# Optimization experiments

Hardware: AMD Instinct MI355X
Metric: run time of the kernel (lower is better)

Reference implementation:

```python
import jax, jax.numpy as jnp
import numpy as np
import math

B = 32; N = 512000; D = 64; NENT = 100000; NEDGE = 1000000; NREL = 200
K_SOURCE = 100; K_MIN = 50; K_MAX = 1000; L_INFL = 4; A_SLOPE = 1.0
TEMP = 1.0; LAM_NOISE = 1.0; COS_EPS = 1e-8


def compute_topk(l):
    # sigmoid schedule for layer-dependent Top-K (python ints, trace-time)
    if l < L_INFL:
        s = 1.0 / (1.0 + math.exp(-A_SLOPE * (l - L_INFL / 2)))
        return int(K_SOURCE + (K_MAX - K_SOURCE) * s)
    s = 1.0 / (1.0 + math.exp(-A_SLOPE * (l - 3 * L_INFL / 2)))
    return int(K_MIN + (K_MAX - K_MIN) * (1.0 - s))


def setup_inputs():
    key = jax.random.key(0)
    k = jax.random.split(key, 14)
    i = jnp.arange(N)
    b = i % B                     # batches interleaved -> every batch has diff nodes
    e = (i // B) * 6 + b          # unique entity per (batch, node), max < NENT
    nodes = jnp.stack([b, e], axis=1)
    return {
        "hidden": jax.random.normal(k[0], (N, D), jnp.float32),
        "nodes": nodes,
        "scores": jax.random.uniform(k[1], (N,), jnp.float32) + 0.1,
        "h0": jax.random.normal(k[2], (1, N, D), jnp.float32),
        "alpha": jax.random.normal(k[3], (NEDGE, 1), jnp.float32),
        "hidden_q": jax.random.normal(k[4], (B, D), jnp.float32),
        "q_rel": jax.random.randint(k[5], (B,), 0, 2 * NREL + 1),
        "edges": jax.random.randint(k[6], (NEDGE, 6), 0, N),
        "old_nodes_new_idx": jnp.arange(N // 2),
        "batch_size": B,
        "message": jax.random.normal(k[7], (NEDGE, D), jnp.float32),
        "obj": jax.random.randint(k[8], (NEDGE,), 0, N),
        "alpha_temp": jax.random.normal(k[9], (NEDGE, 1), jnp.float32),
        "l": 2,
        "noise": jax.random.normal(k[10], (N, 3), jnp.float32),
        "mlp_w1": jax.random.normal(k[11], (2 * D, D), jnp.float32) * 0.05,
        "mlp_b1": jnp.zeros((D,), jnp.float32),
        "mlp_w2": jax.random.normal(k[12], (D, D), jnp.float32) * 0.05,
        "mlp_b2": jnp.zeros((D,), jnp.float32),
        "rel_embed": jax.random.normal(k[13], (2 * NREL + 1, D), jnp.float32) * 0.05,
        "expert_emb": jax.random.normal(jax.random.fold_in(key, 1), (3, D), jnp.float32),
        "w_n": jax.random.normal(jax.random.fold_in(key, 2), (D,), jnp.float32) * 0.05,
    }


def _dense_topk_mult(vals, bidx, eidx, diff, K, B_):
    # scatter per-diff-node values into dense [B, n_ent], softmax over entities,
    # top-K hard mask, straight-through multiplier (hard - sg(p) + p) on diff nodes.
    neg = jnp.float32(-jnp.inf)
    dense = jnp.full((B_, NENT), neg, jnp.float32).at[bidx, eidx].set(jnp.where(diff, vals, neg))
    probs = jax.nn.softmax(dense, axis=1)
    _, idx = jax.lax.top_k(probs, K)
    hard = jnp.zeros((B_, NENT), bool).at[jnp.arange(B_)[:, None], idx].set(True)
    p = probs[bidx, eidx]
    h = hard[bidx, eidx].astype(jnp.float32)
    return jnp.where(diff, h - jax.lax.stop_gradient(p) + p, 1.0)


def _forward(hidden, scores, h0, hidden_q, alpha_temp, mlp_w1, mlp_b1, mlp_w2, mlp_b2,
             rel_embed, expert_emb, w_n, nodes, q_rel, edges, old_nodes_new_idx,
             batch_size, noise, l):
    bidx = nodes[:, 0]
    eidx = nodes[:, 1]
    # ---- noisy gate over 3 pruning experts ----
    q_rel_e = rel_embed[q_rel]                                   # [B, D]
    ctx_in = jnp.concatenate([hidden_q[bidx], q_rel_e[bidx]], axis=-1)  # [N, 2D]
    ctx = jax.nn.relu(ctx_in @ mlp_w1 + mlp_b1) @ mlp_w2 + mlp_b2       # [N, D]
    escore = ctx @ expert_emb.T                                  # [N, 3]
    nscale = jax.nn.softplus(ctx @ w_n)[:, None]                 # [N, 1]
    escore = escore + LAM_NOISE * noise * nscale
    weights = jax.nn.softmax(escore / TEMP, axis=-1)             # [N, 3]
    importance = weights.sum(0) / weights.sum()                  # [3], sums to 1
    w = importance  # num_pruning_experts=3: topk over all 3 + renorm is identity

    diff = jnp.ones((N,), bool).at[old_nodes_new_idx].set(False)
    K_l = compute_topk(l)

    # expert 0: score-based pruner
    m0 = _dense_topk_mult(scores, bidx, eidx, diff, K_l, batch_size)

    # expert 1: cosine-similarity pruner (hidden vs query relation embedding)
    qn = q_rel_e[bidx]
    num = (hidden * qn).sum(-1)
    den = jnp.maximum(jnp.linalg.norm(hidden, axis=-1), COS_EPS) * \
          jnp.maximum(jnp.linalg.norm(qn, axis=-1), COS_EPS)
    m1 = _dense_topk_mult(num / den, bidx, eidx, diff, K_l, batch_size)

    # expert 2: alpha pruner -- segment-max of edge attention onto target nodes,
    # softmax over the global node dim, top-K among new nodes only.
    obj_e = edges[:, 5]
    mx = jax.ops.segment_max(alpha_temp[:, 0], obj_e, num_segments=N)
    node_probs = jax.nn.softmax(mx / TEMP)
    masked = jnp.where(diff, node_probs, -1.0)   # probs >= 0, so topk lands on diff
    _, top_i = jax.lax.top_k(masked, K_l)
    hard2 = jnp.zeros((N,), bool).at[top_i].set(True)
    m2 = jnp.where(diff, hard2.astype(jnp.float32) - jax.lax.stop_gradient(node_probs) + node_probs, 1.0)

    # ---- combine: each expert returns the full node set with diff rows rescaled,
    # and the hashed node-id lookup is the identity permutation here, so the
    # index_add combine reduces to a weighted sum of multipliers. ----
    wm = w[0] * m0 + w[1] * m1 + w[2] * m2                        # [N]
    hidden_c = hidden * wm[:, None]
    scores_c = scores * wm
    h0_c = h0 * wm[None, :, None]

    cv = jnp.std(weights, ddof=1) / (weights.mean() + 1e-5)       # torch unbiased std
    L_imp = cv ** 2
    return hidden_c, scores_c, h0_c, L_imp


def reference(hidden, nodes, scores, h0, alpha, hidden_q, q_rel, edges,
              old_nodes_new_idx, batch_size, message, obj, alpha_temp, l, noise,
              mlp_w1, mlp_b1, mlp_w2, mlp_b2, rel_embed, expert_emb, w_n):
    # alpha / message / obj are passed through in the original but unused in the
    # computed path; the final scores!=0 row filter is replaced by keeping the
    # full (zero-preserving) arrays to stay jit-compatible.
    return _forward(hidden, scores, h0, hidden_q, alpha_temp, mlp_w1, mlp_b1,
                    mlp_w2, mlp_b2, rel_embed, expert_emb, w_n, nodes, q_rel,
                    edges, old_nodes_new_idx, batch_size, noise, l)
```

## Files before the change

### kernel.cpp

```cpp
#include <hip/hip_runtime.h>
#include <stdint.h>
#include <math.h>

#define DD 64
#define K_SOURCE_C 100
#define K_MIN_C 50
#define K_MAX_C 1000
#define L_INFL_C 4
#define A_SLOPE_C 1.0
#define COS_EPS_C 1e-8f
#define NBINS 8192
#define CAPC 3584
#define NHB 192
#define NWB 1024

__device__ __forceinline__ uint32_t f2mono(float f) {
    uint32_t u = __float_as_uint(f);
    return (u & 0x80000000u) ? ~u : (u | 0x80000000u);
}

__constant__ int c_shifts[5] = {51, 38, 25, 12, 0};
__constant__ int c_nbits[5]  = {13, 13, 13, 13, 12};

__global__ void initctx_kernel(uint32_t* mx, uint8_t* diff, int* cnt,
                               int* Kp, int* node_cnt, uint32_t* ghist, const int* l_ptr,
                               const float* hidden_q, const int* q_rel, const float* rel_embed,
                               const float* w1, const float* b1, const float* w2, const float* b2,
                               const float* expert_emb, const float* w_n,
                               float* escore, float* nscale, float* qvec, float* qnorm,
                               int N, int B, int nb) {
    int blk = blockIdx.x, t = threadIdx.x;
    if (blk < nb) {
        int i = blk * 256 + t;
        if (i < N) { mx[i] = 0u; diff[i] = 1; }
        if (i < B) cnt[i] = 0;
        if (i < NBINS) ghist[i] = 0u;
        if (i == 0) {
            *node_cnt = 0;
            double l = (double)(*l_ptr);
            int K;
            if (l < (double)L_INFL_C) {
                double s = 1.0 / (1.0 + exp(-A_SLOPE_C * (l - L_INFL_C / 2.0)));
                K = (int)(K_SOURCE_C + (K_MAX_C - K_SOURCE_C) * s);
            } else {
                double s = 1.0 / (1.0 + exp(-A_SLOPE_C * (l - 3.0 * L_INFL_C / 2.0)));
                K = (int)(K_MIN_C + (K_MAX_C - K_MIN_C) * (1.0 - s));
            }
            *Kp = K;
        }
        return;
    }
    int b = blk - nb;
    if (b >= B) return;
    __shared__ float cin[2 * DD];
    __shared__ float h1s[DD];
    float qv = 0.f;
    if (t < DD) {
        int q = q_rel[b];
        qv = rel_embed[(size_t)q * DD + t];
        qvec[b * DD + t] = qv;
        cin[t] = hidden_q[b * DD + t];
        cin[DD + t] = qv;
    }
    __syncthreads();
    if (t < DD) {
        float acc = b1[t];
        for (int j = 0; j < 2 * DD; j++) acc += cin[j] * w1[j * DD + t];
        h1s[t] = fmaxf(acc, 0.f);
    }
    __syncthreads();
    if (t < DD) {
        float c = b2[t];
        for (int j = 0; j < DD; j++) c += h1s[j] * w2[j * DD + t];
        float e0 = c * expert_emb[0 * DD + t];
        float e1 = c * expert_emb[1 * DD + t];
        float e2 = c * expert_emb[2 * DD + t];
        float wn = c * w_n[t];
        float qq = qv * qv;
        for (int m = 32; m >= 1; m >>= 1) {
            e0 += __shfl_xor(e0, m); e1 += __shfl_xor(e1, m); e2 += __shfl_xor(e2, m);
            wn += __shfl_xor(wn, m); qq += __shfl_xor(qq, m);
        }
        if (t == 0) {
            escore[b * 3 + 0] = e0; escore[b * 3 + 1] = e1; escore[b * 3 + 2] = e2;
            nscale[b] = fmaxf(wn, 0.f) + log1pf(expf(-fabsf(wn)));
            qnorm[b] = fmaxf(sqrtf(qq), COS_EPS_C);
        }
    }
}

__global__ void segdiff_kernel(const int* edges, const float* alpha_temp, uint32_t* mx,
                               uint8_t* diff, const int* old_idx,
                               int NE, int n_old, int N, int eb) {
    int blk = blockIdx.x, t = threadIdx.x;
    if (blk < eb) {
        int e = blk * 256 + t;
        if (e < NE) {
            int o = edges[(size_t)e * 6 + 5];
            if (o >= 0 && o < N) atomicMax(&mx[o], f2mono(alpha_temp[e]));
        }
    } else {
        int j = (blk - eb) * 256 + t;
        if (j < n_old) {
            int idx = old_idx[j];
            if (idx >= 0 && idx < N) diff[idx] = 0;
        }
    }
}

__global__ void nodewc_kernel(const float* hidden, const int* nodes, const float* noise,
                              const float* qvec, const float* qnorm,
                              const float* escore, const float* nscale,
                              float* cosvals, double* partials, int N, int B) {
    int t = threadIdx.x;
    int sub = t & 15;
    double s0 = 0, s1 = 0, s2 = 0, sq = 0;
    int ngroups = (N + 15) >> 4;
    for (int g = blockIdx.x; g < ngroups; g += gridDim.x) {
        int node = g * 16 + (t >> 4);
        if (node < N) {
            int b = nodes[2 * node];
            bool bv = (b >= 0 && b < B);
            float4 h4 = *(const float4*)(hidden + (size_t)node * DD + sub * 4);
            float num = 0.f;
            if (bv) {
                float4 q4 = *(const float4*)(qvec + b * DD + sub * 4);
                num = h4.x * q4.x + h4.y * q4.y + h4.z * q4.z + h4.w * q4.w;
            }
            float hs = h4.x * h4.x + h4.y * h4.y + h4.z * h4.z + h4.w * h4.w;
            for (int m = 8; m >= 1; m >>= 1) { num += __shfl_xor(num, m); hs += __shfl_xor(hs, m); }
            if (sub == 0) {
                float qn = bv ? qnorm[b] : COS_EPS_C;
                cosvals[node] = num / (fmaxf(sqrtf(hs), COS_EPS_C) * qn);
                if (bv) {
                    float ns = nscale[b];
                    float e0 = escore[b * 3 + 0] + noise[3 * node + 0] * ns;
                    float e1 = escore[b * 3 + 1] + noise[3 * node + 1] * ns;
                    float e2 = escore[b * 3 + 2] + noise[3 * node + 2] * ns;
                    float mm = fmaxf(e0, fmaxf(e1, e2));
                    float x0 = expf(e0 - mm), x1 = expf(e1 - mm), x2 = expf(e2 - mm);
                    float s = x0 + x1 + x2;
                    x0 /= s; x1 /= s; x2 /= s;
                    s0 += x0; s1 += x1; s2 += x2;
                    sq += (double)x0 * x0 + (double)x1 * x1 + (double)x2 * x2;
                }
            }
        }
    }
    for (int m = 32; m >= 1; m >>= 1) {
        s0 += __shfl_xor(s0, m); s1 += __shfl_xor(s1, m);
        s2 += __shfl_xor(s2, m); sq += __shfl_xor(sq, m);
    }
    __shared__ double red[4][4];
    int wid = t >> 6, lane = t & 63;
    if (lane == 0) { red[wid][0] = s0; red[wid][1] = s1; red[wid][2] = s2; red[wid][3] = sq; }
    __syncthreads();
    if (t == 0) {
        double a0 = 0, a1 = 0, a2 = 0, a3 = 0;
        for (int w = 0; w < 4; w++) { a0 += red[w][0]; a1 += red[w][1]; a2 += red[w][2]; a3 += red[w][3]; }
        partials[blockIdx.x * 4 + 0] = a0;
        partials[blockIdx.x * 4 + 1] = a1;
        partials[blockIdx.x * 4 + 2] = a2;
        partials[blockIdx.x * 4 + 3] = a3;
    }
}

__global__ void compactstats_kernel(const int* nodes, const uint8_t* diff, const float* scores,
                                    const float* cosvals, const uint32_t* mx,
                                    uint64_t* keys0, uint64_t* keys1, uint64_t* nkeys,
                                    int* cnt, int* node_cnt,
                                    const double* partials, float* wvec, float* out_L,
                                    int N, int B, int CAP, int nb) {
    int blk = blockIdx.x, t = threadIdx.x;
    if (blk == nb) {
        double s0 = 0, s1 = 0, s2 = 0, sq = 0;
        for (int i = t; i < NWB; i += 256) {
            s0 += partials[4 * i + 0]; s1 += partials[4 * i + 1];
            s2 += partials[4 * i + 2]; sq += partials[4 * i + 3];
        }
        for (int m = 32; m >= 1; m >>= 1) {
            s0 += __shfl_xor(s0, m); s1 += __shfl_xor(s1, m);
            s2 += __shfl_xor(s2, m); sq += __shfl_xor(sq, m);
        }
        __shared__ double red[4][4];
        int wid = t >> 6, lane = t & 63;
        if (lane == 0) { red[wid][0] = s0; red[wid][1] = s1; red[wid][2] = s2; red[wid][3] = sq; }
        __syncthreads();
        if (t == 0) {
            double c0 = 0, c1 = 0, c2 = 0, S2 = 0;
            for (int w = 0; w < 4; w++) { c0 += red[w][0]; c1 += red[w][1]; c2 += red[w][2]; S2 += red[w][3]; }
            double tot = c0 + c1 + c2;
            wvec[0] = (float)(c0 / tot); wvec[1] = (float)(c1 / tot); wvec[2] = (float)(c2 / tot);
            double n = 3.0 * (double)N;
            double mean = tot / n;
            double var = (S2 - tot * tot / n) / (n - 1.0);
            if (var < 0) var = 0;
            double cv = sqrt(var) / (mean + 1e-5);
            *out_L = (float)(cv * cv);
        }
        return;
    }
    __shared__ int lcnt[64];
    __shared__ int lbase[64];
    __shared__ int nloc_cnt, nloc_base;
    if (t < B) lcnt[t] = 0;
    if (t == 0) nloc_cnt = 0;
    __syncthreads();
    int i = blk * 256 + t;
    int b = -1, loc = 0, nl = 0;
    bool isdiff = (i < N) && diff[i];
    if (isdiff) {
        nl = atomicAdd(&nloc_cnt, 1);
        int bb = nodes[2 * i];
        if (bb >= 0 && bb < B) { b = bb; loc = atomicAdd(&lcnt[b], 1); }
    }
    __syncthreads();
    if (t < B) lbase[t] = lcnt[t] ? atomicAdd(&cnt[t], lcnt[t]) : 0;
    if (t == 0) nloc_base = nloc_cnt ? atomicAdd(node_cnt, nloc_cnt) : 0;
    __syncthreads();
    if (isdiff) {
        nkeys[nloc_base + nl] = ((uint64_t)mx[i] << 32) | (uint64_t)(0xFFFFFFFFu - (uint32_t)i);
        if (b >= 0) {
            int pos = lbase[b] + loc;
            if (pos < CAP) {
                int ei = nodes[2 * i + 1];
                uint64_t tb = (uint64_t)(0xFFFFFFFFu - (uint32_t)ei);
                keys0[(size_t)b * CAP + pos] = ((uint64_t)f2mono(scores[i]) << 32) | tb;
                keys1[(size_t)b * CAP + pos] = ((uint64_t)f2mono(cosvals[i]) << 32) | tb;
            }
        }
    }
}

struct PickScratch { uint32_t wtot[16]; int fd; uint32_t fK; uint32_t total; };

__device__ void block_pick(const uint32_t* hist, int nbins, uint32_t Kr, PickScratch* sc) {
    int t = threadIdx.x;
    int PB = nbins >> 10;
    int lane = t & 63, wid = t >> 6;
    uint32_t csum = 0;
    for (int j = 0; j < PB; j++) csum += hist[PB * t + j];
    uint32_t ssum = csum;
    for (int off = 1; off < 64; off <<= 1) {
        uint32_t v = __shfl_down(ssum, off, 64);
        if (lane + off < 64) ssum += v;
    }
    if (lane == 0) sc->wtot[wid] = ssum;
    if (t == 0) sc->fd = -1;
    __syncthreads();
    uint32_t above = 0, total = 0;
#pragma unroll
    for (int w = 0; w < 16; w++) {
        uint32_t v = sc->wtot[w];
        total += v;
        if (w > wid) above += v;
    }
    uint32_t gcnt = ssum + above - csum;
    int fd = -1; uint32_t fK = 0;
    for (int j = PB - 1; j >= 0; j--) {
        uint32_t h = hist[PB * t + j];
        if (h && gcnt < Kr && gcnt + h >= Kr) { fd = PB * t + j; fK = Kr - gcnt; }
        gcnt += h;
    }
    if (fd >= 0) { sc->fd = fd; sc->fK = fK; }
    if (t == 0) sc->total = total;
    __syncthreads();
}

__global__ __launch_bounds__(1024)
void selA_kernel(const uint64_t* keys0, const uint64_t* keys1, const int* cnt,
                 const uint64_t* nkeys, const int* node_cnt, uint32_t* ghist,
                 uint64_t* T, const int* Kp, int B, int CAP) {
    __shared__ uint32_t hist[NBINS];
    __shared__ PickScratch sc;
    int t = threadIdx.x;
    int blk = blockIdx.x;
    if (blk < 2 * B) {
        int row = (blk < B) ? blk : blk - B;
        const uint64_t* list = ((blk < B) ? keys0 : keys1) + (size_t)row * CAP;
        int n = min(cnt[row], CAP);
        int K = *Kp;
        if (n <= K) { if (t == 0) T[blk] = 0ull; return; }
        uint64_t pref = 0ull;
        uint32_t Kr = (uint32_t)K;
        for (int lev = 0; lev < 5; lev++) {
            int nb = 1 << c_nbits[lev];
            for (int j = t; j < nb; j += 1024) hist[j] = 0;
            __syncthreads();
            uint64_t pmask = (lev == 0) ? 0ull : (~0ull << c_shifts[lev - 1]);
            int sh = c_shifts[lev];
            uint32_t bmask = (uint32_t)(nb - 1);
            for (int i = t; i < n; i += 1024) {
                uint64_t key = list[i];
                if ((key & pmask) == pref)
                    atomicAdd(&hist[(uint32_t)(key >> sh) & bmask], 1u);
            }
            __syncthreads();
            block_pick(hist, nb, Kr, &sc);
            if (sc.fd < 0) { if (t == 0) T[blk] = 0ull; return; }
            pref |= ((uint64_t)sc.fd) << sh;
            Kr = sc.fK;
            __syncthreads();
        }
        if (t == 0) T[blk] = pref;
    } else {
        int nb = blk - 2 * B;
        for (int j = t; j < NBINS; j += 1024) hist[j] = 0;
        __syncthreads();
        int n = *node_cnt;
        for (int i = nb * 1024 + t; i < n; i += NHB * 1024)
            atomicAdd(&hist[(uint32_t)(nkeys[i] >> 51)], 1u);
        __syncthreads();
        for (int j = t; j < NBINS; j += 1024) {
            uint32_t v = hist[j];
            if (v) atomicAdd(&ghist[j], v);
        }
    }
}

__global__ __launch_bounds__(1024)
void selB_kernel(const uint64_t* nkeys, const int* node_cnt, const uint32_t* ghist,
                 uint64_t* T, const int* Kp, int B) {
    __shared__ uint32_t hist[NBINS];
    __shared__ uint64_t cand[CAPC];
    __shared__ PickScratch sc;
    __shared__ int ccnt;
    int t = threadIdx.x;
    int K = *Kp;
    int n = *node_cnt;
    for (int j = t; j < NBINS; j += 1024) hist[j] = ghist[j];
    __syncthreads();
    block_pick(hist, NBINS, (uint32_t)K, &sc);
    if (sc.total <= (uint32_t)K || sc.fd < 0) { if (t == 0) T[2 * B] = 0ull; return; }
    int fd0 = sc.fd;
    uint64_t pref = ((uint64_t)fd0) << 51;
    uint32_t Kr = sc.fK;
    if (t == 0) ccnt = 0;
    __syncthreads();
    for (int i = t; i < n; i += 1024) {
        uint64_t key = nkeys[i];
        if ((int)(key >> 51) == fd0) {
            int p = atomicAdd(&ccnt, 1);
            if (p < CAPC) cand[p] = key;
        }
    }
    __syncthreads();
    int m = ccnt;
    bool inlds = (m <= CAPC);
    if (!inlds) m = n;
    for (int lev = 1; lev < 5; lev++) {
        int nb = 1 << c_nbits[lev];
        for (int j = t; j < nb; j += 1024) hist[j] = 0;
        __syncthreads();
        uint64_t pmask = ~0ull << c_shifts[lev - 1];
        int sh = c_shifts[lev];
        uint32_t bmask = (uint32_t)(nb - 1);
        for (int i = t; i < m; i += 1024) {
            uint64_t key = inlds ? cand[i] : nkeys[i];
            if ((key & pmask) == pref)
                atomicAdd(&hist[(uint32_t)(key >> sh) & bmask], 1u);
        }
        __syncthreads();
        block_pick(hist, nb, Kr, &sc);
        if (sc.fd < 0) { if (t == 0) T[2 * B] = 0ull; return; }
        pref |= ((uint64_t)sc.fd) << sh;
        Kr = sc.fK;
        __syncthreads();
    }
    if (t == 0) T[2 * B] = pref;
}

__global__ void final_kernel(const float* hidden, const float* h0, const float* scores,
                             const int* nodes, const uint8_t* diff, const float* cosvals,
                             const uint32_t* mx, const uint64_t* T, const float* wvec,
                             float* out_hidden, float* out_scores, float* out_h0,
                             int N, int B) {
    int t = threadIdx.x;
    int node = blockIdx.x * 16 + (t >> 4);
    int sub = t & 15;
    bool ok = node < N;
    float wm = 0.f;
    float sc0 = 0.f;
    if (ok && sub == 0) {
        float w0 = wvec[0], w1 = wvec[1], w2 = wvec[2];
        sc0 = scores[node];
        if (!diff[node]) {
            wm = w0 + w1 + w2;
        } else {
            int b = nodes[2 * node];
            int ei = nodes[2 * node + 1];
            float m0 = 0.f, m1 = 0.f;
            if (b >= 0 && b < B) {
                uint64_t tb = (uint64_t)(0xFFFFFFFFu - (uint32_t)ei);
                uint64_t k0 = ((uint64_t)f2mono(sc0) << 32) | tb;
                uint64_t k1 = ((uint64_t)f2mono(cosvals[node]) << 32) | tb;
                m0 = (k0 >= T[b]) ? 1.f : 0.f;
                m1 = (k1 >= T[B + b]) ? 1.f : 0.f;
            }
            uint64_t k2 = ((uint64_t)mx[node] << 32) | (uint64_t)(0xFFFFFFFFu - (uint32_t)node);
            float m2 = (k2 >= T[2 * B]) ? 1.f : 0.f;
            wm = w0 * m0 + w1 * m1 + w2 * m2;
        }
    }
    wm = __shfl(wm, (t & 63) & ~15, 64);
    if (!ok) return;
    size_t off = (size_t)node * DD + sub * 4;
    float4 h4 = *(const float4*)(hidden + off);
    float4 g4 = *(const float4*)(h0 + off);
    float4 o1, o2;
    o1.x = h4.x * wm; o1.y = h4.y * wm; o1.z = h4.z * wm; o1.w = h4.w * wm;
    o2.x = g4.x * wm; o2.y = g4.y * wm; o2.z = g4.z * wm; o2.w = g4.w * wm;
    *(float4*)(out_hidden + off) = o1;
    *(float4*)(out_h0 + off) = o2;
    if (sub == 0) out_scores[node] = sc0 * wm;
}

extern "C" void kernel_launch(void* const* d_in, const int* in_sizes, int n_in,
                              void* d_out, int out_size, void* d_ws, size_t ws_size,
                              hipStream_t stream) {
    const float* hidden     = (const float*)d_in[0];
    const int*   nodes      = (const int*)d_in[1];
    const float* scores     = (const float*)d_in[2];
    const float* h0         = (const float*)d_in[3];
    const float* hidden_q   = (const float*)d_in[5];
    const int*   q_rel      = (const int*)d_in[6];
    const int*   edges      = (const int*)d_in[7];
    const int*   old_idx    = (const int*)d_in[8];
    const float* alpha_temp = (const float*)d_in[12];
    const int*   l_ptr      = (const int*)d_in[13];
    const float* noise      = (const float*)d_in[14];
    const float* mw1        = (const float*)d_in[15];
    const float* mb1        = (const float*)d_in[16];
    const float* mw2        = (const float*)d_in[17];
    const float* mb2        = (const float*)d_in[18];
    const float* rel_embed  = (const float*)d_in[19];
    const float* expert_emb = (const float*)d_in[20];
    const float* w_n        = (const float*)d_in[21];

    int N     = in_sizes[2];
    int NE    = in_sizes[12];
    int n_old = in_sizes[8];
    int B     = in_sizes[5] / DD;
    int CAP   = N / B;
    int nsel  = 2 * B + 1;

    size_t off = 0;
    auto take = [&](size_t bytes) -> size_t {
        size_t p = off; off += (bytes + 15) & ~(size_t)15; return p;
    };
    char* wsb = (char*)d_ws;
    float*    cosvals  = (float*)   (wsb + take((size_t)N * 4));
    uint32_t* mx       = (uint32_t*)(wsb + take((size_t)N * 4));
    uint8_t*  diff     = (uint8_t*) (wsb + take((size_t)N));
    int*      cnt      = (int*)     (wsb + take((size_t)B * 4));
    double*   partials = (double*)  (wsb + take((size_t)NWB * 4 * 8));
    int*      Kp       = (int*)     (wsb + take(16));
    int*      node_cnt = (int*)     (wsb + take(16));
    float*    escore   = (float*)   (wsb + take((size_t)B * 3 * 4));
    float*    nscale   = (float*)   (wsb + take((size_t)B * 4));
    float*    qvec     = (float*)   (wsb + take((size_t)B * DD * 4));
    float*    qnorm    = (float*)   (wsb + take((size_t)B * 4));
    float*    wvec     = (float*)   (wsb + take(16));
    uint64_t* T        = (uint64_t*)(wsb + take((size_t)nsel * 8));
    uint32_t* ghist    = (uint32_t*)(wsb + take((size_t)NBINS * 4));
    size_t keys_bytes  = (size_t)B * CAP * 8;
    size_t nkeys_bytes = (size_t)N * 8;
    uint64_t *keys0, *keys1, *nkeys;
    if (ws_size >= off + 2 * keys_bytes + nkeys_bytes) {
        keys0 = (uint64_t*)(wsb + take(keys_bytes));
        keys1 = (uint64_t*)(wsb + take(keys_bytes));
        nkeys = (uint64_t*)(wsb + take(nkeys_bytes));
    } else {
        keys0 = (uint64_t*)d_out;
        keys1 = keys0 + (size_t)B * CAP;
        nkeys = keys1 + (size_t)B * CAP;
    }

    float* out_hidden = (float*)d_out;
    float* out_scores = out_hidden + (size_t)N * DD;
    float* out_h0     = out_scores + N;
    float* out_L      = out_h0 + (size_t)N * DD;

    int nb = (N + 255) / 256;
    int eb = (NE + 255) / 256;
    int ob = (n_old + 255) / 256;

    initctx_kernel<<<nb + B, 256, 0, stream>>>(mx, diff, cnt, Kp, node_cnt, ghist, l_ptr,
                                               hidden_q, q_rel, rel_embed, mw1, mb1, mw2, mb2,
                                               expert_emb, w_n, escore, nscale, qvec, qnorm,
                                               N, B, nb);
    segdiff_kernel<<<eb + ob, 256, 0, stream>>>(edges, alpha_temp, mx, diff, old_idx,
                                                NE, n_old, N, eb);
    nodewc_kernel<<<NWB, 256, 0, stream>>>(hidden, nodes, noise, qvec, qnorm,
                                           escore, nscale, cosvals, partials, N, B);
    compactstats_kernel<<<nb + 1, 256, 0, stream>>>(nodes, diff, scores, cosvals, mx,
                                                    keys0, keys1, nkeys, cnt, node_cnt,
                                                    partials, wvec, out_L, N, B, CAP, nb);
    selA_kernel<<<2 * B + NHB, 1024, 0, stream>>>(keys0, keys1, cnt, nkeys, node_cnt,
                                                  ghist, T, Kp, B, CAP);
    selB_kernel<<<1, 1024, 0, stream>>>(nkeys, node_cnt, ghist, T, Kp, B);
    final_kernel<<<(N + 15) / 16, 256, 0, stream>>>(hidden, h0, scores, nodes, diff, cosvals,
                                                    mx, T, wvec, out_hidden, out_scores, out_h0, N, B);
}
```

Before: 823.4 us.

## Merge segdiff into nodewc and fold selB into selA via last-block tail

Merges the edge max/diff-marking kernel with the node cosine/weight kernel into a single prep launch that uses block-range dispatch. It also fuses the two selection kernels: every block increments a done counter, and the last block to finish runs the global-histogram threshold pick. This cuts two kernel launches and the gaps between them. The cost is extra shared memory in the fused selection kernel (the candidate buffer), which may lower occupancy, plus a dependence on threadfence/atomic ordering being correct.

```diff
diff --git a/kernel.cpp b/kernel.cpp
--- a/kernel.cpp
+++ b/kernel.cpp
@@ -23,7 +23,8 @@
 __constant__ int c_nbits[5]  = {13, 13, 13, 13, 12};
 
 __global__ void initctx_kernel(uint32_t* mx, uint8_t* diff, int* cnt,
-                               int* Kp, int* node_cnt, uint32_t* ghist, const int* l_ptr,
+                               int* Kp, int* node_cnt, uint32_t* ghist, uint32_t* done_ctr,
+                               const int* l_ptr,
                                const float* hidden_q, const int* q_rel, const float* rel_embed,
                                const float* w1, const float* b1, const float* w2, const float* b2,
                                const float* expert_emb, const float* w_n,
@@ -37,6 +38,7 @@
         if (i < NBINS) ghist[i] = 0u;
         if (i == 0) {
             *node_cnt = 0;
+            *done_ctr = 0u;
             double l = (double)(*l_ptr);
             int K;
             if (l < (double)L_INFL_C) {
@@ -89,34 +91,35 @@
     }
 }
 
-__global__ void segdiff_kernel(const int* edges, const float* alpha_temp, uint32_t* mx,
-                               uint8_t* diff, const int* old_idx,
-                               int NE, int n_old, int N, int eb) {
+__global__ void prep_kernel(const float* hidden, const int* nodes, const float* noise,
+                            const float* qvec, const float* qnorm,
+                            const float* escore, const float* nscale,
+                            float* cosvals, double* partials,
+                            const int* edges, const float* alpha_temp, uint32_t* mx,
+                            uint8_t* diff, const int* old_idx,
+                            int N, int NE, int n_old, int B, int eb) {
     int blk = blockIdx.x, t = threadIdx.x;
-    if (blk < eb) {
-        int e = blk * 256 + t;
-        if (e < NE) {
-            int o = edges[(size_t)e * 6 + 5];
-            if (o >= 0 && o < N) atomicMax(&mx[o], f2mono(alpha_temp[e]));
-        }
-    } else {
-        int j = (blk - eb) * 256 + t;
-        if (j < n_old) {
-            int idx = old_idx[j];
-            if (idx >= 0 && idx < N) diff[idx] = 0;
-        }
-    }
-}
-
-__global__ void nodewc_kernel(const float* hidden, const int* nodes, const float* noise,
-                              const float* qvec, const float* qnorm,
-                              const float* escore, const float* nscale,
-                              float* cosvals, double* partials, int N, int B) {
-    int t = threadIdx.x;
+    if (blk >= NWB) {
+        int rb = blk - NWB;
+        if (rb < eb) {
+            int e = rb * 256 + t;
+            if (e < NE) {
+                int o = edges[(size_t)e * 6 + 5];
+                if (o >= 0 && o < N) atomicMax(&mx[o], f2mono(alpha_temp[e]));
+            }
+        } else {
+            int j = (rb - eb) * 256 + t;
+            if (j < n_old) {
+                int idx = old_idx[j];
+                if (idx >= 0 && idx < N) diff[idx] = 0;
+            }
+        }
+        return;
+    }
     int sub = t & 15;
     double s0 = 0, s1 = 0, s2 = 0, sq = 0;
     int ngroups = (N + 15) >> 4;
-    for (int g = blockIdx.x; g < ngroups; g += gridDim.x) {
+    for (int g = blk; g < ngroups; g += NWB) {
         int node = g * 16 + (t >> 4);
         if (node < N) {
             int b = nodes[2 * node];
@@ -158,10 +161,10 @@
     if (t == 0) {
         double a0 = 0, a1 = 0, a2 = 0, a3 = 0;
         for (int w = 0; w < 4; w++) { a0 += red[w][0]; a1 += red[w][1]; a2 += red[w][2]; a3 += red[w][3]; }
-        partials[blockIdx.x * 4 + 0] = a0;
-        partials[blockIdx.x * 4 + 1] = a1;
-        partials[blockIdx.x * 4 + 2] = a2;
-        partials[blockIdx.x * 4 + 3] = a3;
+        partials[blk * 4 + 0] = a0;
+        partials[blk * 4 + 1] = a1;
+        partials[blk * 4 + 2] = a2;
+        partials[blk * 4 + 3] = a3;
     }
 }
 
@@ -268,11 +271,14 @@
 }
 
 __global__ __launch_bounds__(1024)
-void selA_kernel(const uint64_t* keys0, const uint64_t* keys1, const int* cnt,
-                 const uint64_t* nkeys, const int* node_cnt, uint32_t* ghist,
-                 uint64_t* T, const int* Kp, int B, int CAP) {
+void selAB_kernel(const uint64_t* keys0, const uint64_t* keys1, const int* cnt,
+                  const uint64_t* nkeys, const int* node_cnt, uint32_t* ghist,
+                  uint64_t* T, const int* Kp, uint32_t* done_ctr, int B, int CAP) {
     __shared__ uint32_t hist[NBINS];
+    __shared__ uint64_t cand[CAPC];
     __shared__ PickScratch sc;
+    __shared__ int ccnt;
+    __shared__ int is_tail;
     int t = threadIdx.x;
     int blk = blockIdx.x;
     if (blk < 2 * B) {
@@ -280,29 +286,34 @@
         const uint64_t* list = ((blk < B) ? keys0 : keys1) + (size_t)row * CAP;
         int n = min(cnt[row], CAP);
         int K = *Kp;
-        if (n <= K) { if (t == 0) T[blk] = 0ull; return; }
-        uint64_t pref = 0ull;
-        uint32_t Kr = (uint32_t)K;
-        for (int lev = 0; lev < 5; lev++) {
-            int nb = 1 << c_nbits[lev];
-            for (int j = t; j < nb; j += 1024) hist[j] = 0;
-            __syncthreads();
-            uint64_t pmask = (lev == 0) ? 0ull : (~0ull << c_shifts[lev - 1]);
-            int sh = c_shifts[lev];
-            uint32_t bmask = (uint32_t)(nb - 1);
-            for (int i = t; i < n; i += 1024) {
-                uint64_t key = list[i];
-                if ((key & pmask) == pref)
-                    atomicAdd(&hist[(uint32_t)(key >> sh) & bmask], 1u);
-            }
-            __syncthreads();
-            block_pick(hist, nb, Kr, &sc);
-            if (sc.fd < 0) { if (t == 0) T[blk] = 0ull; return; }
-            pref |= ((uint64_t)sc.fd) << sh;
-            Kr = sc.fK;
-            __syncthreads();
-        }
-        if (t == 0) T[blk] = pref;
+        if (n <= K) {
+            if (t == 0) T[blk] = 0ull;
+        } else {
+            uint64_t pref = 0ull;
+            uint32_t Kr = (uint32_t)K;
+            bool ok = true;
+            for (int lev = 0; lev < 5; lev++) {
+                if (ok) {
+                    int nb = 1 << c_nbits[lev];
+                    for (int j = t; j < nb; j += 1024) hist[j] = 0;
+                    __syncthreads();
+                    uint64_t pmask = (lev == 0) ? 0ull : (~0ull << c_shifts[lev - 1]);
+                    int sh = c_shifts[lev];
+                    uint32_t bmask = (uint32_t)(nb - 1);
+                    for (int i = t; i < n; i += 1024) {
+                        uint64_t key = list[i];
+                        if ((key & pmask) == pref)
+                            atomicAdd(&hist[(uint32_t)(key >> sh) & bmask], 1u);
+                    }
+                    __syncthreads();
+                    block_pick(hist, nb, Kr, &sc);
+                    if (sc.fd < 0) ok = false;
+                    else { pref |= ((uint64_t)sc.fd) << sh; Kr = sc.fK; }
+                    __syncthreads();
+                }
+            }
+            if (t == 0) T[blk] = ok ? pref : 0ull;
+        }
     } else {
         int nb = blk - 2 * B;
         for (int j = t; j < NBINS; j += 1024) hist[j] = 0;
@@ -316,19 +327,17 @@
             if (v) atomicAdd(&ghist[j], v);
         }
     }
-}
-
-__global__ __launch_bounds__(1024)
-void selB_kernel(const uint64_t* nkeys, const int* node_cnt, const uint32_t* ghist,
-                 uint64_t* T, const int* Kp, int B) {
-    __shared__ uint32_t hist[NBINS];
-    __shared__ uint64_t cand[CAPC];
-    __shared__ PickScratch sc;
-    __shared__ int ccnt;
-    int t = threadIdx.x;
+    __threadfence();
+    __syncthreads();
+    if (t == 0) {
+        uint32_t old = atomicAdd(done_ctr, 1u);
+        is_tail = (old == (uint32_t)(gridDim.x - 1)) ? 1 : 0;
+    }
+    __syncthreads();
+    if (!is_tail) return;
     int K = *Kp;
     int n = *node_cnt;
-    for (int j = t; j < NBINS; j += 1024) hist[j] = ghist[j];
+    for (int j = t; j < NBINS; j += 1024) hist[j] = atomicOr(&ghist[j], 0u);
     __syncthreads();
     block_pick(hist, NBINS, (uint32_t)K, &sc);
     if (sc.total <= (uint32_t)K || sc.fd < 0) { if (t == 0) T[2 * B] = 0ull; return; }
@@ -456,6 +465,7 @@
     double*   partials = (double*)  (wsb + take((size_t)NWB * 4 * 8));
     int*      Kp       = (int*)     (wsb + take(16));
     int*      node_cnt = (int*)     (wsb + take(16));
+    uint32_t* done_ctr = (uint32_t*)(wsb + take(16));
     float*    escore   = (float*)   (wsb + take((size_t)B * 3 * 4));
     float*    nscale   = (float*)   (wsb + take((size_t)B * 4));
     float*    qvec     = (float*)   (wsb + take((size_t)B * DD * 4));
@@ -485,20 +495,19 @@
     int eb = (NE + 255) / 256;
     int ob = (n_old + 255) / 256;
 
-    initctx_kernel<<<nb + B, 256, 0, stream>>>(mx, diff, cnt, Kp, node_cnt, ghist, l_ptr,
-                                               hidden_q, q_rel, rel_embed, mw1, mb1, mw2, mb2,
-                                               expert_emb, w_n, escore, nscale, qvec, qnorm,
-                                               N, B, nb);
-    segdiff_kernel<<<eb + ob, 256, 0, stream>>>(edges, alpha_temp, mx, diff, old_idx,
-                                                NE, n_old, N, eb);
-    nodewc_kernel<<<NWB, 256, 0, stream>>>(hidden, nodes, noise, qvec, qnorm,
-                                           escore, nscale, cosvals, partials, N, B);
+    initctx_kernel<<<nb + B, 256, 0, stream>>>(mx, diff, cnt, Kp, node_cnt, ghist, done_ctr,
+                                               l_ptr, hidden_q, q_rel, rel_embed,
+                                               mw1, mb1, mw2, mb2, expert_emb, w_n,
+                                               escore, nscale, qvec, qnorm, N, B, nb);
+    prep_kernel<<<NWB + eb + ob, 256, 0, stream>>>(hidden, nodes, noise, qvec, qnorm,
+                                                   escore, nscale, cosvals, partials,
+                                                   edges, alpha_temp, mx, diff, old_idx,
+                                                   N, NE, n_old, B, eb);
     compactstats_kernel<<<nb + 1, 256, 0, stream>>>(nodes, diff, scores, cosvals, mx,
                                                     keys0, keys1, nkeys, cnt, node_cnt,
                                                     partials, wvec, out_L, N, B, CAP, nb);
-    selA_kernel<<<2 * B + NHB, 1024, 0, stream>>>(keys0, keys1, cnt, nkeys, node_cnt,
-                                                  ghist, T, Kp, B, CAP);
-    selB_kernel<<<1, 1024, 0, stream>>>(nkeys, node_cnt, ghist, T, Kp, B);
+    selAB_kernel<<<2 * B + NHB, 1024, 0, stream>>>(keys0, keys1, cnt, nkeys, node_cnt,
+                                                   ghist, T, Kp, done_ctr, B, CAP);
     final_kernel<<<(N + 15) / 16, 256, 0, stream>>>(hidden, h0, scores, nodes, diff, cosvals,
                                                     mx, T, wvec, out_hidden, out_scores, out_h0, N, B);
 }
```

Result: slower. 864.8 us (+5.0%).
